# Performance work log

Hardware: AMD Instinct MI355X
Metric: run time of the kernel (lower is better)

Reference implementation:

```python
import jax, jax.numpy as jnp
import numpy as np

N_I = 500_000   # 'indivi' nodes (dst)
N_H = 200_000   # 'house' nodes
F_I = 32        # indivi feature dim
F_H = 16        # house feature dim
EF = 8          # edge_attr dim
E1 = 2_000_000  # house->indivi edges
E2 = 2_000_000  # indivi->indivi edges


def setup_inputs() -> dict:
    key = jax.random.key(0)
    ks = jax.random.split(key, 16)
    return {
        "x_indivi": jax.random.normal(ks[0], (N_I, F_I), jnp.float32),
        "x_house": jax.random.normal(ks[1], (N_H, F_H), jnp.float32),
        "edge_attr_h2i": jax.random.normal(ks[2], (E1, EF), jnp.float32),
        "edge_attr_i2i": jax.random.normal(ks[3], (E2, EF), jnp.float32),
        "W_edge_h2i": jax.random.normal(ks[4], (F_H, EF), jnp.float32) * 0.1,
        "b_edge_h2i": jax.random.normal(ks[5], (F_H,), jnp.float32) * 0.1,
        "W_edge_i2i": jax.random.normal(ks[6], (F_I, EF), jnp.float32) * 0.1,
        "b_edge_i2i": jax.random.normal(ks[7], (F_I,), jnp.float32) * 0.1,
        "W_root_h2i": jax.random.normal(ks[8], (1, F_I), jnp.float32) * 0.1,
        "bias_h2i": jax.random.normal(ks[9], (1,), jnp.float32) * 0.1,
        "W_root_i2i": jax.random.normal(ks[10], (1, F_I), jnp.float32) * 0.1,
        "bias_i2i": jax.random.normal(ks[11], (1,), jnp.float32) * 0.1,
        "src_h2i": jax.random.randint(ks[12], (E1,), 0, N_H, jnp.int32),
        "dst_h2i": jax.random.randint(ks[13], (E1,), 0, N_I, jnp.int32),
        "src_i2i": jax.random.randint(ks[14], (E2,), 0, N_I, jnp.int32),
        "dst_i2i": jax.random.randint(ks[15], (E2,), 0, N_I, jnp.int32),
    }


def _nnconv(x_src, x_dst, edge_attr, src, dst, W_edge, b_edge, W_root, bias, num_dst):
    # Edge MLP -> per-edge weight matrix of shape [F_src, out=1], flattened to [E, F_src]
    w = edge_attr @ W_edge.T + b_edge                     # [E, F_src]
    # message_e = x_src[src_e] @ w_e  (out_channels = 1)
    msg = jnp.sum(x_src[src] * w, axis=-1, keepdims=True)  # [E, 1]
    agg = jax.ops.segment_sum(msg, dst, num_segments=num_dst)  # [N_dst, 1]
    # root transform on destination features + bias
    return agg + x_dst @ W_root.T + bias                  # [N_dst, 1]


def reference(x_indivi, x_house, edge_attr_h2i, edge_attr_i2i,
              W_edge_h2i, b_edge_h2i, W_edge_i2i, b_edge_i2i,
              W_root_h2i, bias_h2i, W_root_i2i, bias_i2i,
              src_h2i, dst_h2i, src_i2i, dst_i2i):
    out_h = _nnconv(x_house, x_indivi, edge_attr_h2i, src_h2i, dst_h2i,
                    W_edge_h2i, b_edge_h2i, W_root_h2i, bias_h2i, N_I)
    out_i = _nnconv(x_indivi, x_indivi, edge_attr_i2i, src_i2i, dst_i2i,
                    W_edge_i2i, b_edge_i2i, W_root_i2i, bias_i2i, N_I)
    # HeteroConv(aggr='sum') over the two relations targeting 'indivi'
    return out_h + out_i
```

## Files before the change

### kernel.cpp

```cpp
#include <hip/hip_runtime.h>

#define N_I 500000
#define N_H 200000
#define E1  2000000
#define E2  2000000
#define TOTAL_E (E1 + E2)

#define BSHIFT 12
#define NB 128
#define NBK ((N_I + 4095) / 4096)
#define CHUNK 2048
#define NWG ((TOTAL_E + CHUNK - 1) / CHUNK)
#define WPT 8
#define ITERS (CHUNK / 256)

typedef float f4 __attribute__((ext_vector_type(4)));

template<int F, bool ROOT>
__global__ __launch_bounds__(256) void precompute_g(
    const float* __restrict__ x, const float* __restrict__ W, const float* __restrict__ b,
    uint4* __restrict__ g8, _Float16* __restrict__ gc, int n,
    const float* __restrict__ rW1, const float* __restrict__ rW2,
    const float* __restrict__ rb1, const float* __restrict__ rb2,
    float* __restrict__ out)
{
    __shared__ float Wf[F * 8];
    __shared__ float bv[F];
    __shared__ float wr[F];

    for (int i = threadIdx.x; i < F * 8; i += 256) Wf[i] = W[i];
    if (threadIdx.x < F) {
        bv[threadIdx.x] = b[threadIdx.x];
        if (ROOT) wr[threadIdx.x] = rW1[threadIdx.x] + rW2[threadIdx.x];
    }
    __syncthreads();

    int nid = blockIdx.x * 256 + threadIdx.x;
    if (nid >= n) return;

    float xv[F];
    const f4* xp = (const f4*)(x + (size_t)nid * F);
    #pragma unroll
    for (int q = 0; q < F / 4; q++) {
        f4 v = __builtin_nontemporal_load(xp + q);
        xv[q*4+0] = v[0]; xv[q*4+1] = v[1]; xv[q*4+2] = v[2]; xv[q*4+3] = v[3];
    }

    float acc[9];
    #pragma unroll
    for (int k = 0; k < 9; k++) acc[k] = 0.f;

    #pragma unroll
    for (int j = 0; j < F; j++) {
        float4 w0 = *(const float4*)(Wf + j * 8);
        float4 w1 = *(const float4*)(Wf + j * 8 + 4);
        float xj = xv[j];
        acc[0] = fmaf(xj, w0.x, acc[0]);
        acc[1] = fmaf(xj, w0.y, acc[1]);
        acc[2] = fmaf(xj, w0.z, acc[2]);
        acc[3] = fmaf(xj, w0.w, acc[3]);
        acc[4] = fmaf(xj, w1.x, acc[4]);
        acc[5] = fmaf(xj, w1.y, acc[5]);
        acc[6] = fmaf(xj, w1.z, acc[6]);
        acc[7] = fmaf(xj, w1.w, acc[7]);
        acc[8] = fmaf(xj, bv[j], acc[8]);
    }

    union { _Float16 h[8]; uint4 u; } pk;
    #pragma unroll
    for (int k = 0; k < 8; k++) pk.h[k] = (_Float16)acc[k];
    g8[nid] = pk.u;
    gc[nid] = (_Float16)acc[8];

    if (ROOT) {
        float r = rb1[0] + rb2[0];
        #pragma unroll
        for (int j = 0; j < F; j++) r = fmaf(xv[j], wr[j], r);
        out[nid] = r;
    }
}

__global__ __launch_bounds__(256) void hist_kernel(
    const int* __restrict__ dst1, const int* __restrict__ dst2,
    int* __restrict__ H)
{
    __shared__ int hist[NB];
    if (threadIdx.x < NB) hist[threadIdx.x] = 0;
    __syncthreads();

    int base = blockIdx.x * CHUNK;
    #pragma unroll
    for (int it = 0; it < ITERS; ++it) {
        int t = base + it * 256 + threadIdx.x;
        if (t < TOTAL_E) {
            int d = (t < E1) ? __builtin_nontemporal_load(&dst1[t])
                             : __builtin_nontemporal_load(&dst2[t - E1]);
            atomicAdd(&hist[d >> BSHIFT], 1);
        }
    }
    __syncthreads();
    if (threadIdx.x < NB) H[blockIdx.x * NB + threadIdx.x] = hist[threadIdx.x];
}

__global__ __launch_bounds__(256) void scan_cols_kernel(int* __restrict__ H,
                                                        int* __restrict__ total)
{
    __shared__ int sums[256];
    int b = blockIdx.x;
    int tid = threadIdx.x;

    int vals[WPT];
    int s = 0;
    #pragma unroll
    for (int k = 0; k < WPT; k++) {
        int w = tid * WPT + k;
        vals[k] = (w < NWG) ? H[w * NB + b] : 0;
        s += vals[k];
    }
    sums[tid] = s;
    __syncthreads();
    for (int off = 1; off < 256; off <<= 1) {
        int t = (tid >= off) ? sums[tid - off] : 0;
        __syncthreads();
        sums[tid] += t;
        __syncthreads();
    }
    int run = sums[tid] - s;
    #pragma unroll
    for (int k = 0; k < WPT; k++) {
        int w = tid * WPT + k;
        if (w < NWG) H[w * NB + b] = run;
        run += vals[k];
    }
    if (tid == 255) total[b] = sums[255];
}

__global__ __launch_bounds__(128) void scan_base_kernel(const int* __restrict__ total,
                                                        int* __restrict__ base)
{
    __shared__ int v[NB];
    int tid = threadIdx.x;
    int orig = total[tid];
    v[tid] = orig;
    __syncthreads();
    for (int off = 1; off < NB; off <<= 1) {
        int t = (tid >= off) ? v[tid - off] : 0;
        __syncthreads();
        v[tid] += t;
        __syncthreads();
    }
    base[tid] = v[tid] - orig;
}

__device__ __forceinline__ float msg_dot(uint4 gu, f4 a0, f4 a1, float base) {
    union { uint4 u; _Float16 h[8]; } pk; pk.u = gu;
    float m = base;
    m = fmaf((float)pk.h[0], a0[0], m);
    m = fmaf((float)pk.h[1], a0[1], m);
    m = fmaf((float)pk.h[2], a0[2], m);
    m = fmaf((float)pk.h[3], a0[3], m);
    m = fmaf((float)pk.h[4], a1[0], m);
    m = fmaf((float)pk.h[5], a1[1], m);
    m = fmaf((float)pk.h[6], a1[2], m);
    m = fmaf((float)pk.h[7], a1[3], m);
    return m;
}

__device__ __forceinline__ void compute_msgs8(
    int tid, int ebase,
    const int* __restrict__ src, const int* __restrict__ dst,
    const float* __restrict__ ea, const uint4* __restrict__ g8,
    const _Float16* __restrict__ gc,
    int* dloc, float* mloc)
{
    int sl[ITERS];
    #pragma unroll
    for (int it = 0; it < ITERS; ++it) {
        int e = ebase + it * 256 + tid;
        sl[it] = __builtin_nontemporal_load(&src[e]);
        dloc[it] = __builtin_nontemporal_load(&dst[e]);
    }
    #pragma unroll
    for (int h = 0; h < 2; ++h) {
        uint4 g[4]; f4 a0[4], a1[4];
        float gv[4];
        #pragma unroll
        for (int k = 0; k < 4; ++k) {
            int it = h * 4 + k;
            int e = ebase + it * 256 + tid;
            int s = sl[it];
            g[k] = g8[s];
            gv[k] = (float)gc[s];
            const f4* ap = (const f4*)(ea + (size_t)e * 8);
            a0[k] = __builtin_nontemporal_load(ap);
            a1[k] = __builtin_nontemporal_load(ap + 1);
        }
        #pragma unroll
        for (int k = 0; k < 4; ++k)
            mloc[h * 4 + k] = msg_dot(g[k], a0[k], a1[k], gv[k]);
    }
}

__global__ __launch_bounds__(256) void scatter_fused_kernel(
    const int* __restrict__ src1, const int* __restrict__ dst1,
    const float* __restrict__ ea1, const uint4* __restrict__ g8_1, const _Float16* __restrict__ gc_1,
    const int* __restrict__ src2, const int* __restrict__ dst2,
    const float* __restrict__ ea2, const uint4* __restrict__ g8_2, const _Float16* __restrict__ gc_2,
    const int* __restrict__ H, const int* __restrict__ base,
    float* __restrict__ msgs_out, unsigned short* __restrict__ lidx_out)
{
    __shared__ int cnt[NB];
    __shared__ int sv[NB];
    __shared__ int gbase[NB];
    __shared__ unsigned int lu[CHUNK];
    __shared__ float lm[CHUNK];

    int tid = threadIdx.x;
    if (tid < NB) cnt[tid] = 0;
    __syncthreads();

    int cbase = blockIdx.x * CHUNK;
    int dloc[ITERS];
    float mloc[ITERS];

    if (cbase + CHUNK <= E1) {
        compute_msgs8(tid, cbase, src1, dst1, ea1, g8_1, gc_1, dloc, mloc);
    } else if (cbase >= E1 && cbase + CHUNK <= TOTAL_E) {
        compute_msgs8(tid, cbase - E1, src2, dst2, ea2, g8_2, gc_2, dloc, mloc);
    } else {
        #pragma unroll
        for (int it = 0; it < ITERS; ++it) {
            int t = cbase + it * 256 + tid;
            int d = -1; float m = 0.f;
            if (t < TOTAL_E) {
                const int* srcp; const int* dstp; const float* eap;
                const uint4* g8p; const _Float16* gcp; int e;
                if (t < E1) { e = t;      srcp = src1; dstp = dst1; eap = ea1; g8p = g8_1; gcp = gc_1; }
                else        { e = t - E1; srcp = src2; dstp = dst2; eap = ea2; g8p = g8_2; gcp = gc_2; }
                int s = srcp[e];
                d = dstp[e];
                uint4 gu = g8p[s];
                const f4* ap = (const f4*)(eap + (size_t)e * 8);
                f4 a0 = ap[0];
                f4 a1 = ap[1];
                m = msg_dot(gu, a0, a1, (float)gcp[s]);
            }
            dloc[it] = d; mloc[it] = m;
        }
    }

    #pragma unroll
    for (int it = 0; it < ITERS; ++it)
        if (dloc[it] >= 0) atomicAdd(&cnt[dloc[it] >> BSHIFT], 1);
    __syncthreads();

    int myc = 0;
    if (tid < NB) { myc = cnt[tid]; sv[tid] = myc; }
    __syncthreads();
    for (int off = 1; off < NB; off <<= 1) {
        int t = (tid < NB && tid >= off) ? sv[tid - off] : 0;
        __syncthreads();
        if (tid < NB) sv[tid] += t;
        __syncthreads();
    }
    if (tid < NB) {
        int loff = sv[tid] - myc;
        gbase[tid] = H[blockIdx.x * NB + tid] + base[tid] - loff;
        cnt[tid] = loff;
    }
    __syncthreads();

    #pragma unroll
    for (int it = 0; it < ITERS; ++it) {
        int d = dloc[it];
        if (d >= 0) {
            int b = d >> BSHIFT;
            int slot = atomicAdd(&cnt[b], 1);
            lu[slot] = ((unsigned)b << BSHIFT) | (unsigned)(d & 4095);
            lm[slot] = mloc[it];
        }
    }
    __syncthreads();

    int nvalid = TOTAL_E - cbase;
    if (nvalid > CHUNK) nvalid = CHUNK;
    for (int i = tid; i < nvalid; i += 256) {
        unsigned u = lu[i];
        int b = (int)(u >> BSHIFT);
        int g = gbase[b] + i;
        __builtin_nontemporal_store(lm[i], &msgs_out[g]);
        __builtin_nontemporal_store((unsigned short)(u & 4095u), &lidx_out[g]);
    }
}

__global__ __launch_bounds__(512) void reduce_atomic_kernel(
    const float* __restrict__ msgs, const unsigned short* __restrict__ lidx,
    const int* __restrict__ base, const int* __restrict__ total,
    float* __restrict__ out)
{
    __shared__ float acc[4096];
    for (int i = threadIdx.x; i < 4096; i += 512) acc[i] = 0.f;
    __syncthreads();

    int b = blockIdx.x >> 2;
    int k = blockIdx.x & 3;
    int start = base[b];
    int cnt = total[b];
    int q = (cnt + 3) >> 2;
    int s0 = k * q;
    int s1 = s0 + q; if (s1 > cnt) s1 = cnt;

    for (int i = s0 + threadIdx.x; i < s1; i += 512) {
        unsigned short li = __builtin_nontemporal_load(&lidx[start + i]);
        float mv = __builtin_nontemporal_load(&msgs[start + i]);
        atomicAdd(&acc[li], mv);
    }
    __syncthreads();

    int node0 = b << BSHIFT;
    for (int i = threadIdx.x; i < 4096; i += 512) {
        float v = acc[i];
        int n = node0 + i;
        if (v != 0.f && n < N_I) atomicAdd(out + n, v);
    }
}

__global__ __launch_bounds__(256) void edge_kernel_atomic(
    const int* __restrict__ src1, const int* __restrict__ dst1,
    const float* __restrict__ ea1, const uint4* __restrict__ g8_1, const _Float16* __restrict__ gc_1,
    const int* __restrict__ src2, const int* __restrict__ dst2,
    const float* __restrict__ ea2, const uint4* __restrict__ g8_2, const _Float16* __restrict__ gc_2,
    float* __restrict__ out)
{
    int t = blockIdx.x * 256 + threadIdx.x;
    if (t >= TOTAL_E) return;
    const int* srcp; const int* dstp; const float* eap;
    const uint4* g8p; const _Float16* gcp; int e;
    if (t < E1) { e = t;      srcp = src1; dstp = dst1; eap = ea1; g8p = g8_1; gcp = gc_1; }
    else        { e = t - E1; srcp = src2; dstp = dst2; eap = ea2; g8p = g8_2; gcp = gc_2; }
    int s = srcp[e];
    int d = dstp[e];
    uint4 gu = g8p[s];
    const f4* ap = (const f4*)(eap + (size_t)e * 8);
    f4 a0 = ap[0];
    f4 a1 = ap[1];
    float m = msg_dot(gu, a0, a1, (float)gcp[s]);
    atomicAdd(out + d, m);
}

extern "C" void kernel_launch(void* const* d_in, const int* in_sizes, int n_in,
                              void* d_out, int out_size, void* d_ws, size_t ws_size,
                              hipStream_t stream) {
    const float* x_i  = (const float*)d_in[0];
    const float* x_h  = (const float*)d_in[1];
    const float* ea_h = (const float*)d_in[2];
    const float* ea_i = (const float*)d_in[3];
    const float* We_h = (const float*)d_in[4];
    const float* be_h = (const float*)d_in[5];
    const float* We_i = (const float*)d_in[6];
    const float* be_i = (const float*)d_in[7];
    const float* Wr_h = (const float*)d_in[8];
    const float* br_h = (const float*)d_in[9];
    const float* Wr_i = (const float*)d_in[10];
    const float* br_i = (const float*)d_in[11];
    const int* src_h = (const int*)d_in[12];
    const int* dst_h = (const int*)d_in[13];
    const int* src_i = (const int*)d_in[14];
    const int* dst_i = (const int*)d_in[15];

    float* out = (float*)d_out;

    char* ws = (char*)d_ws;
    uint4*    g8_i = (uint4*)ws;
    uint4*    g8_h = (uint4*)(ws + 8000000);
    _Float16* gc_i = (_Float16*)(ws + 11200000);
    _Float16* gc_h = (_Float16*)(ws + 12200000);
    float*    msgs = (float*)(ws + 12800000);
    unsigned short* lidx = (unsigned short*)(ws + 28800000);
    int*      H    = (int*)(ws + 36800000);
    int*      tot  = (int*)(ws + 37800448);
    int*      bas  = (int*)(ws + 37800960);
    const size_t WS_NEEDED = 37801472;

    precompute_g<16, false><<<(N_H + 255) / 256, 256, 0, stream>>>(
        x_h, We_h, be_h, g8_h, gc_h, N_H, nullptr, nullptr, nullptr, nullptr, nullptr);
    precompute_g<32, true><<<(N_I + 255) / 256, 256, 0, stream>>>(
        x_i, We_i, be_i, g8_i, gc_i, N_I, Wr_h, Wr_i, br_h, br_i, out);

    if (ws_size >= WS_NEEDED) {
        hist_kernel<<<NWG, 256, 0, stream>>>(dst_h, dst_i, H);
        scan_cols_kernel<<<NB, 256, 0, stream>>>(H, tot);
        scan_base_kernel<<<1, NB, 0, stream>>>(tot, bas);
        scatter_fused_kernel<<<NWG, 256, 0, stream>>>(
            src_h, dst_h, ea_h, g8_h, gc_h,
            src_i, dst_i, ea_i, g8_i, gc_i,
            H, bas, msgs, lidx);
        reduce_atomic_kernel<<<NBK * 4, 512, 0, stream>>>(msgs, lidx, bas, tot, out);
    } else {
        edge_kernel_atomic<<<(TOTAL_E + 255) / 256, 256, 0, stream>>>(
            src_h, dst_h, ea_h, g8_h, gc_h,
            src_i, dst_i, ea_i, g8_i, gc_i, out);
    }
}
```

Before: 366.0 us.

## Replace bucketed scatter-reduce pipeline with direct global atomics and fuse precompute

Removes the histogram, scan, bucket-sort scatter and shared-memory reduce kernels and instead has the edge kernel atomically add each message directly to the output. The two per-node precompute kernels are merged into one launch split by block index. This aims to cut launch count and the intermediate message/index buffer traffic, at the cost of millions of scattered global float atomics that may contend in L2.

```diff
diff --git a/kernel.cpp b/kernel.cpp
--- a/kernel.cpp
+++ b/kernel.cpp
@@ -6,36 +6,33 @@
 #define E2  2000000
 #define TOTAL_E (E1 + E2)
 
-#define BSHIFT 12
-#define NB 128
-#define NBK ((N_I + 4095) / 4096)
 #define CHUNK 2048
 #define NWG ((TOTAL_E + CHUNK - 1) / CHUNK)
-#define WPT 8
 #define ITERS (CHUNK / 256)
 
+#define NBI_BLK ((N_I + 255) / 256)
+#define NBH_BLK ((N_H + 255) / 256)
+
 typedef float f4 __attribute__((ext_vector_type(4)));
 
 template<int F, bool ROOT>
-__global__ __launch_bounds__(256) void precompute_g(
+__device__ __forceinline__ void precompute_body(
+    int blk, int tid,
     const float* __restrict__ x, const float* __restrict__ W, const float* __restrict__ b,
     uint4* __restrict__ g8, _Float16* __restrict__ gc, int n,
     const float* __restrict__ rW1, const float* __restrict__ rW2,
     const float* __restrict__ rb1, const float* __restrict__ rb2,
-    float* __restrict__ out)
-{
-    __shared__ float Wf[F * 8];
-    __shared__ float bv[F];
-    __shared__ float wr[F];
-
-    for (int i = threadIdx.x; i < F * 8; i += 256) Wf[i] = W[i];
-    if (threadIdx.x < F) {
-        bv[threadIdx.x] = b[threadIdx.x];
-        if (ROOT) wr[threadIdx.x] = rW1[threadIdx.x] + rW2[threadIdx.x];
+    float* __restrict__ out,
+    float* Wf, float* bv, float* wr)
+{
+    for (int i = tid; i < F * 8; i += 256) Wf[i] = W[i];
+    if (tid < F) {
+        bv[tid] = b[tid];
+        if (ROOT) wr[tid] = rW1[tid] + rW2[tid];
     }
     __syncthreads();
 
-    int nid = blockIdx.x * 256 + threadIdx.x;
+    int nid = blk * 256 + tid;
     if (nid >= n) return;
 
     float xv[F];
@@ -80,76 +77,27 @@
     }
 }
 
-__global__ __launch_bounds__(256) void hist_kernel(
-    const int* __restrict__ dst1, const int* __restrict__ dst2,
-    int* __restrict__ H)
-{
-    __shared__ int hist[NB];
-    if (threadIdx.x < NB) hist[threadIdx.x] = 0;
-    __syncthreads();
-
-    int base = blockIdx.x * CHUNK;
-    #pragma unroll
-    for (int it = 0; it < ITERS; ++it) {
-        int t = base + it * 256 + threadIdx.x;
-        if (t < TOTAL_E) {
-            int d = (t < E1) ? __builtin_nontemporal_load(&dst1[t])
-                             : __builtin_nontemporal_load(&dst2[t - E1]);
-            atomicAdd(&hist[d >> BSHIFT], 1);
-        }
-    }
-    __syncthreads();
-    if (threadIdx.x < NB) H[blockIdx.x * NB + threadIdx.x] = hist[threadIdx.x];
-}
-
-__global__ __launch_bounds__(256) void scan_cols_kernel(int* __restrict__ H,
-                                                        int* __restrict__ total)
-{
-    __shared__ int sums[256];
-    int b = blockIdx.x;
-    int tid = threadIdx.x;
-
-    int vals[WPT];
-    int s = 0;
-    #pragma unroll
-    for (int k = 0; k < WPT; k++) {
-        int w = tid * WPT + k;
-        vals[k] = (w < NWG) ? H[w * NB + b] : 0;
-        s += vals[k];
-    }
-    sums[tid] = s;
-    __syncthreads();
-    for (int off = 1; off < 256; off <<= 1) {
-        int t = (tid >= off) ? sums[tid - off] : 0;
-        __syncthreads();
-        sums[tid] += t;
-        __syncthreads();
-    }
-    int run = sums[tid] - s;
-    #pragma unroll
-    for (int k = 0; k < WPT; k++) {
-        int w = tid * WPT + k;
-        if (w < NWG) H[w * NB + b] = run;
-        run += vals[k];
-    }
-    if (tid == 255) total[b] = sums[255];
-}
-
-__global__ __launch_bounds__(128) void scan_base_kernel(const int* __restrict__ total,
-                                                        int* __restrict__ base)
-{
-    __shared__ int v[NB];
-    int tid = threadIdx.x;
-    int orig = total[tid];
-    v[tid] = orig;
-    __syncthreads();
-    for (int off = 1; off < NB; off <<= 1) {
-        int t = (tid >= off) ? v[tid - off] : 0;
-        __syncthreads();
-        v[tid] += t;
-        __syncthreads();
-    }
-    base[tid] = v[tid] - orig;
+__global__ __launch_bounds__(256) void precompute_both(
+    const float* __restrict__ x_i, const float* __restrict__ We_i, const float* __restrict__ be_i,
+    uint4* __restrict__ g8_i, _Float16* __restrict__ gc_i,
+    const float* __restrict__ x_h, const float* __restrict__ We_h, const float* __restrict__ be_h,
+    uint4* __restrict__ g8_h, _Float16* __restrict__ gc_h,
+    const float* __restrict__ rW1, const float* __restrict__ rW2,
+    const float* __restrict__ rb1, const float* __restrict__ rb2,
+    float* __restrict__ out)
+{
+    __shared__ float Wf[32 * 8];
+    __shared__ float bv[32];
+    __shared__ float wr[32];
+
+    if (blockIdx.x < NBI_BLK) {
+        precompute_body<32, true>(blockIdx.x, threadIdx.x, x_i, We_i, be_i,
+                                  g8_i, gc_i, N_I, rW1, rW2, rb1, rb2, out, Wf, bv, wr);
+    } else {
+        precompute_body<16, false>(blockIdx.x - NBI_BLK, threadIdx.x, x_h, We_h, be_h,
+                                   g8_h, gc_h, N_H, nullptr, nullptr, nullptr, nullptr,
+                                   nullptr, Wf, bv, wr);
+    }
 }
 
 __device__ __forceinline__ float msg_dot(uint4 gu, f4 a0, f4 a1, float base) {
@@ -201,24 +149,14 @@
     }
 }
 
-__global__ __launch_bounds__(256) void scatter_fused_kernel(
+__global__ __launch_bounds__(256) void edge_atomic_kernel(
     const int* __restrict__ src1, const int* __restrict__ dst1,
     const float* __restrict__ ea1, const uint4* __restrict__ g8_1, const _Float16* __restrict__ gc_1,
     const int* __restrict__ src2, const int* __restrict__ dst2,
     const float* __restrict__ ea2, const uint4* __restrict__ g8_2, const _Float16* __restrict__ gc_2,
-    const int* __restrict__ H, const int* __restrict__ base,
-    float* __restrict__ msgs_out, unsigned short* __restrict__ lidx_out)
-{
-    __shared__ int cnt[NB];
-    __shared__ int sv[NB];
-    __shared__ int gbase[NB];
-    __shared__ unsigned int lu[CHUNK];
-    __shared__ float lm[CHUNK];
-
+    float* __restrict__ out)
+{
     int tid = threadIdx.x;
-    if (tid < NB) cnt[tid] = 0;
-    __syncthreads();
-
     int cbase = blockIdx.x * CHUNK;
     int dloc[ITERS];
     float mloc[ITERS];
@@ -251,101 +189,7 @@
 
     #pragma unroll
     for (int it = 0; it < ITERS; ++it)
-        if (dloc[it] >= 0) atomicAdd(&cnt[dloc[it] >> BSHIFT], 1);
-    __syncthreads();
-
-    int myc = 0;
-    if (tid < NB) { myc = cnt[tid]; sv[tid] = myc; }
-    __syncthreads();
-    for (int off = 1; off < NB; off <<= 1) {
-        int t = (tid < NB && tid >= off) ? sv[tid - off] : 0;
-        __syncthreads();
-        if (tid < NB) sv[tid] += t;
-        __syncthreads();
-    }
-    if (tid < NB) {
-        int loff = sv[tid] - myc;
-        gbase[tid] = H[blockIdx.x * NB + tid] + base[tid] - loff;
-        cnt[tid] = loff;
-    }
-    __syncthreads();
-
-    #pragma unroll
-    for (int it = 0; it < ITERS; ++it) {
-        int d = dloc[it];
-        if (d >= 0) {
-            int b = d >> BSHIFT;
-            int slot = atomicAdd(&cnt[b], 1);
-            lu[slot] = ((unsigned)b << BSHIFT) | (unsigned)(d & 4095);
-            lm[slot] = mloc[it];
-        }
-    }
-    __syncthreads();
-
-    int nvalid = TOTAL_E - cbase;
-    if (nvalid > CHUNK) nvalid = CHUNK;
-    for (int i = tid; i < nvalid; i += 256) {
-        unsigned u = lu[i];
-        int b = (int)(u >> BSHIFT);
-        int g = gbase[b] + i;
-        __builtin_nontemporal_store(lm[i], &msgs_out[g]);
-        __builtin_nontemporal_store((unsigned short)(u & 4095u), &lidx_out[g]);
-    }
-}
-
-__global__ __launch_bounds__(512) void reduce_atomic_kernel(
-    const float* __restrict__ msgs, const unsigned short* __restrict__ lidx,
-    const int* __restrict__ base, const int* __restrict__ total,
-    float* __restrict__ out)
-{
-    __shared__ float acc[4096];
-    for (int i = threadIdx.x; i < 4096; i += 512) acc[i] = 0.f;
-    __syncthreads();
-
-    int b = blockIdx.x >> 2;
-    int k = blockIdx.x & 3;
-    int start = base[b];
-    int cnt = total[b];
-    int q = (cnt + 3) >> 2;
-    int s0 = k * q;
-    int s1 = s0 + q; if (s1 > cnt) s1 = cnt;
-
-    for (int i = s0 + threadIdx.x; i < s1; i += 512) {
-        unsigned short li = __builtin_nontemporal_load(&lidx[start + i]);
-        float mv = __builtin_nontemporal_load(&msgs[start + i]);
-        atomicAdd(&acc[li], mv);
-    }
-    __syncthreads();
-
-    int node0 = b << BSHIFT;
-    for (int i = threadIdx.x; i < 4096; i += 512) {
-        float v = acc[i];
-        int n = node0 + i;
-        if (v != 0.f && n < N_I) atomicAdd(out + n, v);
-    }
-}
-
-__global__ __launch_bounds__(256) void edge_kernel_atomic(
-    const int* __restrict__ src1, const int* __restrict__ dst1,
-    const float* __restrict__ ea1, const uint4* __restrict__ g8_1, const _Float16* __restrict__ gc_1,
-    const int* __restrict__ src2, const int* __restrict__ dst2,
-    const float* __restrict__ ea2, const uint4* __restrict__ g8_2, const _Float16* __restrict__ gc_2,
-    float* __restrict__ out)
-{
-    int t = blockIdx.x * 256 + threadIdx.x;
-    if (t >= TOTAL_E) return;
-    const int* srcp; const int* dstp; const float* eap;
-    const uint4* g8p; const _Float16* gcp; int e;
-    if (t < E1) { e = t;      srcp = src1; dstp = dst1; eap = ea1; g8p = g8_1; gcp = gc_1; }
-    else        { e = t - E1; srcp = src2; dstp = dst2; eap = ea2; g8p = g8_2; gcp = gc_2; }
-    int s = srcp[e];
-    int d = dstp[e];
-    uint4 gu = g8p[s];
-    const f4* ap = (const f4*)(eap + (size_t)e * 8);
-    f4 a0 = ap[0];
-    f4 a1 = ap[1];
-    float m = msg_dot(gu, a0, a1, (float)gcp[s]);
-    atomicAdd(out + d, m);
+        if (dloc[it] >= 0) atomicAdd(out + dloc[it], mloc[it]);
 }
 
 extern "C" void kernel_launch(void* const* d_in, const int* in_sizes, int n_in,
@@ -375,30 +219,13 @@
     uint4*    g8_h = (uint4*)(ws + 8000000);
     _Float16* gc_i = (_Float16*)(ws + 11200000);
     _Float16* gc_h = (_Float16*)(ws + 12200000);
-    float*    msgs = (float*)(ws + 12800000);
-    unsigned short* lidx = (unsigned short*)(ws + 28800000);
-    int*      H    = (int*)(ws + 36800000);
-    int*      tot  = (int*)(ws + 37800448);
-    int*      bas  = (int*)(ws + 37800960);
-    const size_t WS_NEEDED = 37801472;
-
-    precompute_g<16, false><<<(N_H + 255) / 256, 256, 0, stream>>>(
-        x_h, We_h, be_h, g8_h, gc_h, N_H, nullptr, nullptr, nullptr, nullptr, nullptr);
-    precompute_g<32, true><<<(N_I + 255) / 256, 256, 0, stream>>>(
-        x_i, We_i, be_i, g8_i, gc_i, N_I, Wr_h, Wr_i, br_h, br_i, out);
-
-    if (ws_size >= WS_NEEDED) {
-        hist_kernel<<<NWG, 256, 0, stream>>>(dst_h, dst_i, H);
-        scan_cols_kernel<<<NB, 256, 0, stream>>>(H, tot);
-        scan_base_kernel<<<1, NB, 0, stream>>>(tot, bas);
-        scatter_fused_kernel<<<NWG, 256, 0, stream>>>(
-            src_h, dst_h, ea_h, g8_h, gc_h,
-            src_i, dst_i, ea_i, g8_i, gc_i,
-            H, bas, msgs, lidx);
-        reduce_atomic_kernel<<<NBK * 4, 512, 0, stream>>>(msgs, lidx, bas, tot, out);
-    } else {
-        edge_kernel_atomic<<<(TOTAL_E + 255) / 256, 256, 0, stream>>>(
-            src_h, dst_h, ea_h, g8_h, gc_h,
-            src_i, dst_i, ea_i, g8_i, gc_i, out);
-    }
-}
+
+    precompute_both<<<NBI_BLK + NBH_BLK, 256, 0, stream>>>(
+        x_i, We_i, be_i, g8_i, gc_i,
+        x_h, We_h, be_h, g8_h, gc_h,
+        Wr_h, Wr_i, br_h, br_i, out);
+
+    edge_atomic_kernel<<<NWG, 256, 0, stream>>>(
+        src_h, dst_h, ea_h, g8_h, gc_h,
+        src_i, dst_i, ea_i, g8_i, gc_i, out);
+}
```

New measurement: 441.5 us. 20.6% more time.
